# Kernel tuning notes

Hardware: AMD Instinct MI355X
Metric: run time of the kernel (lower is better)

## Reference

```python
import jax, jax.numpy as jnp
import numpy as np

B, S, E, H, FF, NQ = 8, 2048, 768, 96, 3072, 128
D_K = E // H  # 8
EPS = 1e-5


def _layernorm(x, g, b):
    m = jnp.mean(x, axis=-1, keepdims=True)
    v = jnp.mean(jnp.square(x - m), axis=-1, keepdims=True)
    return (x - m) * jax.lax.rsqrt(v + EPS) * g + b


def setup_inputs() -> dict:
    key = jax.random.key(0)
    ks = jax.random.split(key, 6)
    sc = 0.02
    return {
        "x": jax.random.normal(ks[0], (B, S, E), jnp.float32),
        "Wp": jax.random.normal(ks[1], (E, E), jnp.float32) * sc,
        "theta_rx": jax.random.normal(ks[2], (E,), jnp.float32) * sc,
        "theta_ry": jax.random.normal(ks[3], (NQ,), jnp.float32) * sc,
        "W1": jax.random.normal(ks[4], (FF, NQ), jnp.float32) * sc,
        "b1": jnp.zeros((FF,), jnp.float32),
        "W2": jax.random.normal(ks[5], (E, FF), jnp.float32) * sc,
        "b2": jnp.zeros((E,), jnp.float32),
        "ln1_g": jnp.ones((E,), jnp.float32),
        "ln1_b": jnp.zeros((E,), jnp.float32),
        "ln2_g": jnp.ones((E,), jnp.float32),
        "ln2_b": jnp.zeros((E,), jnp.float32),
    }


def reference(x, Wp, theta_rx, theta_ry, W1, b1, W2, b2, ln1_g, ln1_b, ln2_g, ln2_b):
    # --- QAttention ---
    proj = jnp.einsum('bse,fe->bsf', x, Wp)            # nn.Linear(E,E,bias=False)
    # RX(x) then RX(theta) on |0>, <Z> = cos(x+theta): batched across tokens
    qa = jnp.cos(proj + theta_rx)                      # [B,S,E]
    scores = jnp.einsum('bsd,btd->bst', qa, qa) / jnp.sqrt(jnp.float32(D_K))
    attn = jax.nn.softmax(scores, axis=-1)             # dropout=0 (eval)
    attn_out = jnp.einsum('bst,btd->bsd', attn, qa)    # [B,S,E]
    x1 = _layernorm(x + attn_out, ln1_g, ln1_b)
    # --- QFeedForward ---
    # RY(x) then RY(theta) on |0>, <Z> = cos(x+theta); encoder reads first NQ feats
    qf = jnp.cos(x1[..., :NQ] + theta_ry)              # [B,S,NQ]
    h = jax.nn.relu(jnp.einsum('bsq,fq->bsf', qf, W1) + b1)
    ffn_out = jnp.einsum('bsf,ef->bse', h, W2) + b2
    return _layernorm(x1 + ffn_out, ln2_g, ln2_b)
```

## Files before the change

kernel.cpp:

```cpp
#include <hip/hip_runtime.h>
#include <hip/hip_bf16.h>
#include <cstdio>
#include <cstdint>

typedef __bf16 bf16x8 __attribute__((ext_vector_type(8)));
typedef unsigned short u16;
typedef u16 u16x8 __attribute__((ext_vector_type(8)));
typedef float f32x4 __attribute__((ext_vector_type(4)));

#define DEV __device__ __forceinline__

static constexpr int B_ = 8, S_ = 2048, E_ = 768, NQ_ = 128, FF_ = 3072;
static constexpr int BS_ = B_ * S_;

DEV u16 f2b(float f) {
    unsigned u = __builtin_bit_cast(unsigned, f);
    unsigned r = (u + 0x7fffu + ((u >> 16) & 1u)) >> 16;
    return (u16)r;
}

#define GLD16(gp, lp) __builtin_amdgcn_global_load_lds( \
    (const __attribute__((address_space(1))) void*)(gp), \
    (__attribute__((address_space(3))) void*)(lp), 16, 0, 0)

__global__ void cvt_bf16(const float* __restrict__ in, u16* __restrict__ out, int n)
{
    const int stride = gridDim.x * blockDim.x * 4;
    for (int i = (blockIdx.x * blockDim.x + threadIdx.x) * 4; i < n; i += stride) {
        const float4 f = *(const float4*)(in + i);
        ushort4 u;
        u.x = f2b(f.x); u.y = f2b(f.y); u.z = f2b(f.z); u.w = f2b(f.w);
        *(ushort4*)(out + i) = u;
    }
}

template<int K>
DEV void kstage(const u16* A, const u16* Bm, u16* As, u16* Bs,
                int m0, int n0, int k0, int w, int t)
{
    #pragma unroll
    for (int r = 0; r < 4; ++r) {
        const int ci = r * 512 + t;
        const int row = ci >> 3;
        const int colb = ((ci & 7) * 16) ^ ((row & 7) << 4);
        GLD16(A  + (size_t)(m0 + row) * K + k0 + (colb >> 1),
              As + (size_t)(r * 512 + w * 64) * 8);
        GLD16(Bm + (size_t)(n0 + row) * K + k0 + (colb >> 1),
              Bs + (size_t)(r * 512 + w * 64) * 8);
    }
}

template<bool FIRST>
DEV void kcompute(const u16* As, const u16* Bs, f32x4 (&acc)[8][4],
                  int wr, int wc, int lane)
{
    #pragma unroll
    for (int kk = 0; kk < 2; ++kk) {
        bf16x8 af[8], bf[4];
        const int cb = kk * 64 + ((lane >> 4) << 4);
        #pragma unroll
        for (int m = 0; m < 8; ++m) {
            const int row = wr * 128 + m * 16 + (lane & 15);
            af[m] = *(const bf16x8*)((const char*)As + row * 128 + (cb ^ ((row & 7) << 4)));
        }
        #pragma unroll
        for (int n = 0; n < 4; ++n) {
            const int row = wc * 64 + n * 16 + (lane & 15);
            bf[n] = *(const bf16x8*)((const char*)Bs + row * 128 + (cb ^ ((row & 7) << 4)));
        }
        #pragma unroll
        for (int m = 0; m < 8; ++m)
            #pragma unroll
            for (int n = 0; n < 4; ++n) {
                if (FIRST && kk == 0)
                    asm("v_mfma_f32_16x16x32_bf16 %0, %1, %2, 0"
                        : "=a"(acc[m][n]) : "v"(af[m]), "v"(bf[n]));
                else
                    asm("v_mfma_f32_16x16x32_bf16 %0, %1, %2, %0"
                        : "+a"(acc[m][n]) : "v"(af[m]), "v"(bf[n]));
            }
    }
}

template<int K, int MODE>
__global__ __launch_bounds__(512, 2)
void gemm_bt(const u16* __restrict__ A, const u16* __restrict__ Bm,
             const float* __restrict__ bias, void* __restrict__ out, int N,
             size_t sA, size_t sB, size_t sC)
{
    __shared__ u16 lds[4 * 256 * 64];
    const int t = threadIdx.x;
    const int w = t >> 6, lane = t & 63;
    const int m0 = blockIdx.x * 256, n0 = blockIdx.y * 256;
    const int wr = w >> 2, wc = w & 3;
    A  += (size_t)blockIdx.z * sA;
    Bm += (size_t)blockIdx.z * sB;
    u16*   ob16 = (u16*)out   + (size_t)blockIdx.z * sC;
    float* of32 = (float*)out + (size_t)blockIdx.z * sC;
    f32x4 acc[8][4];

    kstage<K>(A, Bm, lds, lds + 16384, m0, n0, 0, w, t);
    __syncthreads();
    int cur = 0;
    for (int k0 = 0; k0 < K; k0 += 64) {
        const int nxt = cur ^ 32768;
        if (k0 + 64 < K)
            kstage<K>(A, Bm, lds + nxt, lds + nxt + 16384, m0, n0, k0 + 64, w, t);
        if (k0 == 0) kcompute<true >(lds + cur, lds + cur + 16384, acc, wr, wc, lane);
        else         kcompute<false>(lds + cur, lds + cur + 16384, acc, wr, wc, lane);
        __syncthreads();
        cur = nxt;
    }

    __builtin_amdgcn_sched_barrier(0);
    asm volatile("s_nop 7\n\ts_nop 7");
    __builtin_amdgcn_sched_barrier(0);

    #pragma unroll
    for (int m = 0; m < 8; ++m) {
        const int rowb = m0 + wr * 128 + m * 16 + ((lane >> 4) << 2);
        #pragma unroll
        for (int n = 0; n < 4; ++n) {
            const int col = n0 + wc * 64 + n * 16 + (lane & 15);
            float bv = 0.f;
            if (MODE == 0 || MODE == 1 || MODE == 2) bv = bias[col];
            #pragma unroll
            for (int r = 0; r < 4; ++r) {
                const float c = acc[m][n][r];
                const size_t idx = (size_t)(rowb + r) * N + col;
                if (MODE == 0)      ob16[idx] = f2b(__cosf(c + bv));
                else if (MODE == 1) ob16[idx] = f2b(fmaxf(c + bv, 0.f));
                else if (MODE == 2) of32[idx] = c + bv;
                else if (MODE == 3) of32[idx] = c;
                else                of32[idx] = c * 0.35355339059327373f;
            }
        }
    }
}

__global__ __launch_bounds__(256)
void transpose_bf16(const u16* __restrict__ in, u16* __restrict__ outp)
{
    __shared__ u16 tile[64][72];
    const int b = blockIdx.z;
    const int s0 = blockIdx.x * 64, d0 = blockIdx.y * 64;
    const int t = threadIdx.x;
    const u16* src = in + ((size_t)b * S_ + s0) * E_ + d0;
    #pragma unroll
    for (int i = 0; i < 2; ++i) {
        const int r = (t >> 3) + i * 32;
        const int c = (t & 7) * 8;
        u16x8 v = *(const u16x8*)(src + (size_t)r * E_ + c);
        #pragma unroll
        for (int e = 0; e < 8; ++e) tile[r][c + e] = v[e];
    }
    __syncthreads();
    u16* dst = outp + ((size_t)b * E_ + d0) * S_ + s0;
    #pragma unroll
    for (int i = 0; i < 2; ++i) {
        const int r = (t >> 3) + i * 32;
        const int c = (t & 7) * 8;
        u16x8 v;
        #pragma unroll
        for (int e = 0; e < 8; ++e) v[e] = tile[c + e][r];
        *(u16x8*)(dst + (size_t)r * S_ + c) = v;
    }
}

__global__ __launch_bounds__(256)
void softmax_rows(const float* __restrict__ s, u16* __restrict__ pout)
{
    const int t = threadIdx.x;
    const float* row = s + (size_t)blockIdx.x * (size_t)S_;
    float f[8];
    {
        const float4 a = *(const float4*)(row + t * 8);
        const float4 b = *(const float4*)(row + t * 8 + 4);
        f[0] = a.x; f[1] = a.y; f[2] = a.z; f[3] = a.w;
        f[4] = b.x; f[5] = b.y; f[6] = b.z; f[7] = b.w;
    }
    float mx = f[0];
    #pragma unroll
    for (int e = 1; e < 8; ++e) mx = fmaxf(mx, f[e]);
    #pragma unroll
    for (int d = 1; d < 64; d <<= 1) mx = fmaxf(mx, __shfl_xor(mx, d));
    __shared__ float sh[8];
    if ((t & 63) == 0) sh[t >> 6] = mx;
    __syncthreads();
    mx = fmaxf(fmaxf(sh[0], sh[1]), fmaxf(sh[2], sh[3]));
    float sum = 0.f;
    #pragma unroll
    for (int e = 0; e < 8; ++e) { f[e] = __expf(f[e] - mx); sum += f[e]; }
    #pragma unroll
    for (int d = 1; d < 64; d <<= 1) sum += __shfl_xor(sum, d);
    if ((t & 63) == 0) sh[4 + (t >> 6)] = sum;
    __syncthreads();
    sum = sh[4] + sh[5] + sh[6] + sh[7];
    const float inv = 1.f / sum;
    u16x8 v;
    #pragma unroll
    for (int e = 0; e < 8; ++e) v[e] = f2b(f[e] * inv);
    *(u16x8*)(pout + (size_t)blockIdx.x * (size_t)S_ + t * 8) = v;
}

__global__ __launch_bounds__(256)
void ln_fuse(const float* __restrict__ a, const float* __restrict__ res,
             const float* __restrict__ g, const float* __restrict__ bb,
             const float* __restrict__ theta, float* __restrict__ out,
             u16* __restrict__ qf)
{
    const int row = blockIdx.x, t = threadIdx.x;
    const float* ar = a + (size_t)row * E_;
    const float* rr = res + (size_t)row * E_;
    float v0 = ar[t] + rr[t];
    float v1 = ar[t + 256] + rr[t + 256];
    float v2 = ar[t + 512] + rr[t + 512];
    float s1 = v0 + v1 + v2;
    float s2 = v0 * v0 + v1 * v1 + v2 * v2;
    #pragma unroll
    for (int d = 1; d < 64; d <<= 1) { s1 += __shfl_xor(s1, d); s2 += __shfl_xor(s2, d); }
    __shared__ float sh[8];
    if ((t & 63) == 0) { sh[t >> 6] = s1; sh[4 + (t >> 6)] = s2; }
    __syncthreads();
    s1 = sh[0] + sh[1] + sh[2] + sh[3];
    s2 = sh[4] + sh[5] + sh[6] + sh[7];
    const float mean = s1 * (1.f / 768.f);
    const float var = s2 * (1.f / 768.f) - mean * mean;
    const float rs = rsqrtf(var + 1e-5f);
    float* orow = out + (size_t)row * E_;
    const float y0 = (v0 - mean) * rs * g[t] + bb[t];
    const float y1 = (v1 - mean) * rs * g[t + 256] + bb[t + 256];
    const float y2 = (v2 - mean) * rs * g[t + 512] + bb[t + 512];
    orow[t] = y0; orow[t + 256] = y1; orow[t + 512] = y2;
    if (qf != nullptr && t < NQ_)
        qf[(size_t)row * NQ_ + t] = f2b(cosf(y0 + theta[t]));
}

extern "C" void kernel_launch(void* const* d_in, const int* in_sizes, int n_in,
                              void* d_out, int out_size, void* d_ws, size_t ws_size,
                              hipStream_t stream)
{
    (void)in_sizes; (void)n_in; (void)out_size;
    const float* x    = (const float*)d_in[0];
    const float* Wp   = (const float*)d_in[1];
    const float* trx  = (const float*)d_in[2];
    const float* try_ = (const float*)d_in[3];
    const float* W1   = (const float*)d_in[4];
    const float* b1   = (const float*)d_in[5];
    const float* W2   = (const float*)d_in[6];
    const float* b2   = (const float*)d_in[7];
    const float* g1   = (const float*)d_in[8];
    const float* bb1  = (const float*)d_in[9];
    const float* g2   = (const float*)d_in[10];
    const float* bb2  = (const float*)d_in[11];
    float* out = (float*)d_out;

    const size_t MiB = (size_t)1 << 20;
    char* arena = (char*)d_ws;
    u16*   x_b    = (u16*)  (arena + 0);
    u16*   Wp_b   = (u16*)  (arena + 24 * MiB);
    u16*   qa     = (u16*)  (arena + 128 * MiB);
    u16*   qaT    = (u16*)  (arena + 192 * MiB);
    float* scores = (float*)(arena + 0);
    u16*   probs  = (u16*)  (arena + 128 * MiB);
    float* ao     = (float*)(arena + 0);
    float* x1     = (float*)(arena + 144 * MiB);
    u16*   qf     = (u16*)  (arena + 192 * MiB);
    u16*   h      = (u16*)  (arena + 48 * MiB);
    u16*   W1_b   = (u16*)  (arena + 216 * MiB);
    u16*   W2_b   = (u16*)  (arena + 216 * MiB + (size_t)FF_ * NQ_ * 2);
    const size_t need = 216 * MiB + (size_t)FF_ * NQ_ * 2 + (size_t)E_ * FF_ * 2;
    if (need > ws_size) {
        fprintf(stderr, "kernel_launch: ws too small: need=%zu have=%zu\n", need, ws_size);
        return;
    }

    cvt_bf16<<<512, 256, 0, stream>>>(x,  x_b,  BS_ * E_);
    cvt_bf16<<<64,  256, 0, stream>>>(Wp, Wp_b, E_ * E_);
    cvt_bf16<<<64,  256, 0, stream>>>(W1, W1_b, FF_ * NQ_);
    cvt_bf16<<<64,  256, 0, stream>>>(W2, W2_b, E_ * FF_);

    gemm_bt<E_, 0><<<dim3(BS_ / 256, E_ / 256), 512, 0, stream>>>(
        x_b, Wp_b, trx, qa, E_, 0, 0, 0);
    transpose_bf16<<<dim3(S_ / 64, E_ / 64, B_), 256, 0, stream>>>(qa, qaT);
    gemm_bt<E_, 4><<<dim3(S_ / 256, S_ / 256, B_), 512, 0, stream>>>(
        qa, qa, nullptr, scores, S_,
        (size_t)S_ * E_, (size_t)S_ * E_, (size_t)S_ * S_);
    softmax_rows<<<BS_, 256, 0, stream>>>(scores, probs);
    gemm_bt<S_, 3><<<dim3(S_ / 256, E_ / 256, B_), 512, 0, stream>>>(
        probs, qaT, nullptr, ao, E_,
        (size_t)S_ * S_, (size_t)E_ * S_, (size_t)S_ * E_);

    ln_fuse<<<BS_, 256, 0, stream>>>(ao, x, g1, bb1, try_, x1, qf);
    gemm_bt<NQ_, 1><<<dim3(BS_ / 256, FF_ / 256), 512, 0, stream>>>(
        qf, W1_b, b1, h, FF_, 0, 0, 0);
    gemm_bt<FF_, 2><<<dim3(BS_ / 256, E_ / 256), 512, 0, stream>>>(
        h, W2_b, b2, ao, E_, 0, 0, 0);
    ln_fuse<<<BS_, 256, 0, stream>>>(ao, x1, g2, bb2, nullptr, out, nullptr);
}
```

Baseline: 415.1 us.

## Switch GEMM mainloop to triple-buffered BK=32 stages with explicit vmcnt waits

Replaces the double-buffered BK=64 LDS pipeline with a three-stage ring of BK=32 tiles. Prefetch runs two stages ahead, and explicit s_waitcnt vmcnt(4) lets the next stage's global-to-LDS loads stay in flight. The swizzle is redone for 64-byte rows. LDS use drops from 128KB to 96KB per block, which may help occupancy. The cost is two barriers per half-size k-step, which doubles synchronisation relative to the MFMA work done between barriers.

```diff
diff --git a/kernel.cpp b/kernel.cpp
--- a/kernel.cpp
+++ b/kernel.cpp
@@ -35,51 +35,51 @@
 }
 
 template<int K>
-DEV void kstage(const u16* A, const u16* Bm, u16* As, u16* Bs,
-                int m0, int n0, int k0, int w, int t)
-{
-    #pragma unroll
-    for (int r = 0; r < 4; ++r) {
+DEV void kstage32(const u16* A, const u16* Bm, u16* As, u16* Bs,
+                  int m0, int n0, int k0, int w, int t)
+{
+    #pragma unroll
+    for (int r = 0; r < 2; ++r) {
         const int ci = r * 512 + t;
-        const int row = ci >> 3;
-        const int colb = ((ci & 7) * 16) ^ ((row & 7) << 4);
-        GLD16(A  + (size_t)(m0 + row) * K + k0 + (colb >> 1),
+        const int row = ci >> 2;
+        const int sw = (row & 3) ^ ((row >> 2) & 3);
+        const int cu = ((ci & 3) ^ sw) * 8;
+        GLD16(A  + (size_t)(m0 + row) * K + k0 + cu,
               As + (size_t)(r * 512 + w * 64) * 8);
-        GLD16(Bm + (size_t)(n0 + row) * K + k0 + (colb >> 1),
+        GLD16(Bm + (size_t)(n0 + row) * K + k0 + cu,
               Bs + (size_t)(r * 512 + w * 64) * 8);
     }
 }
 
 template<bool FIRST>
-DEV void kcompute(const u16* As, const u16* Bs, f32x4 (&acc)[8][4],
-                  int wr, int wc, int lane)
-{
-    #pragma unroll
-    for (int kk = 0; kk < 2; ++kk) {
-        bf16x8 af[8], bf[4];
-        const int cb = kk * 64 + ((lane >> 4) << 4);
-        #pragma unroll
-        for (int m = 0; m < 8; ++m) {
-            const int row = wr * 128 + m * 16 + (lane & 15);
-            af[m] = *(const bf16x8*)((const char*)As + row * 128 + (cb ^ ((row & 7) << 4)));
-        }
+DEV void kcompute32(const u16* As, const u16* Bs, f32x4 (&acc)[8][4],
+                    int wr, int wc, int lane)
+{
+    bf16x8 af[8], bf[4];
+    const int cb = (lane >> 4) << 4;
+    #pragma unroll
+    for (int m = 0; m < 8; ++m) {
+        const int row = wr * 128 + m * 16 + (lane & 15);
+        const int sw = ((row & 3) ^ ((row >> 2) & 3)) << 4;
+        af[m] = *(const bf16x8*)((const char*)As + row * 64 + (cb ^ sw));
+    }
+    #pragma unroll
+    for (int n = 0; n < 4; ++n) {
+        const int row = wc * 64 + n * 16 + (lane & 15);
+        const int sw = ((row & 3) ^ ((row >> 2) & 3)) << 4;
+        bf[n] = *(const bf16x8*)((const char*)Bs + row * 64 + (cb ^ sw));
+    }
+    #pragma unroll
+    for (int m = 0; m < 8; ++m)
         #pragma unroll
         for (int n = 0; n < 4; ++n) {
-            const int row = wc * 64 + n * 16 + (lane & 15);
-            bf[n] = *(const bf16x8*)((const char*)Bs + row * 128 + (cb ^ ((row & 7) << 4)));
+            if (FIRST)
+                asm("v_mfma_f32_16x16x32_bf16 %0, %1, %2, 0"
+                    : "=a"(acc[m][n]) : "v"(af[m]), "v"(bf[n]));
+            else
+                asm("v_mfma_f32_16x16x32_bf16 %0, %1, %2, %0"
+                    : "+a"(acc[m][n]) : "v"(af[m]), "v"(bf[n]));
         }
-        #pragma unroll
-        for (int m = 0; m < 8; ++m)
-            #pragma unroll
-            for (int n = 0; n < 4; ++n) {
-                if (FIRST && kk == 0)
-                    asm("v_mfma_f32_16x16x32_bf16 %0, %1, %2, 0"
-                        : "=a"(acc[m][n]) : "v"(af[m]), "v"(bf[n]));
-                else
-                    asm("v_mfma_f32_16x16x32_bf16 %0, %1, %2, %0"
-                        : "+a"(acc[m][n]) : "v"(af[m]), "v"(bf[n]));
-            }
-    }
 }
 
 template<int K, int MODE>
@@ -88,7 +88,7 @@
              const float* __restrict__ bias, void* __restrict__ out, int N,
              size_t sA, size_t sB, size_t sC)
 {
-    __shared__ u16 lds[4 * 256 * 64];
+    __shared__ u16 lds[3 * 16384];
     const int t = threadIdx.x;
     const int w = t >> 6, lane = t & 63;
     const int m0 = blockIdx.x * 256, n0 = blockIdx.y * 256;
@@ -99,17 +99,31 @@
     float* of32 = (float*)out + (size_t)blockIdx.z * sC;
     f32x4 acc[8][4];
 
-    kstage<K>(A, Bm, lds, lds + 16384, m0, n0, 0, w, t);
-    __syncthreads();
-    int cur = 0;
-    for (int k0 = 0; k0 < K; k0 += 64) {
-        const int nxt = cur ^ 32768;
-        if (k0 + 64 < K)
-            kstage<K>(A, Bm, lds + nxt, lds + nxt + 16384, m0, n0, k0 + 64, w, t);
-        if (k0 == 0) kcompute<true >(lds + cur, lds + cur + 16384, acc, wr, wc, lane);
-        else         kcompute<false>(lds + cur, lds + cur + 16384, acc, wr, wc, lane);
-        __syncthreads();
-        cur = nxt;
+    const int NS = K / 32;
+    kstage32<K>(A, Bm, lds,         lds + 8192,         m0, n0, 0,  w, t);
+    kstage32<K>(A, Bm, lds + 16384, lds + 16384 + 8192, m0, n0, 32, w, t);
+    asm volatile("s_waitcnt vmcnt(4)" ::: "memory");
+    __builtin_amdgcn_s_barrier();
+    __builtin_amdgcn_sched_barrier(0);
+
+    for (int s = 0; s < NS; ++s) {
+        const int cur = (s % 3) * 16384;
+        if (s + 2 < NS) {
+            const int nx2 = ((s + 2) % 3) * 16384;
+            kstage32<K>(A, Bm, lds + nx2, lds + nx2 + 8192,
+                        m0, n0, (s + 2) * 32, w, t);
+        }
+        if (s == 0) kcompute32<true >(lds + cur, lds + cur + 8192, acc, wr, wc, lane);
+        else        kcompute32<false>(lds + cur, lds + cur + 8192, acc, wr, wc, lane);
+        __builtin_amdgcn_sched_barrier(0);
+        asm volatile("s_waitcnt lgkmcnt(0)" ::: "memory");
+        __builtin_amdgcn_s_barrier();
+        if (s + 2 < NS)
+            asm volatile("s_waitcnt vmcnt(4)" ::: "memory");
+        else
+            asm volatile("s_waitcnt vmcnt(0)" ::: "memory");
+        __builtin_amdgcn_s_barrier();
+        __builtin_amdgcn_sched_barrier(0);
     }
 
     __builtin_amdgcn_sched_barrier(0);
```

Result: slower. 438.4 us (+5.6%).

## Shrink GEMM tiles to 128x128 single-buffered, keep 256 tile for W1 GEMM

Applied to the files above, without the earlier changes.

The generic GEMM now uses 128x128 tiles with 4 waves, 256 threads and single-buffered LDS with two barriers per k-step, replacing the 256x256 double-buffered design. It is used for the Wp, QK^T, PV and W2 GEMMs. A copy of the old 256-tile kernel is kept only for the short-K W1 GEMM. The goal is more blocks and better occupancy and tail balance on small grids, at the cost of less reuse per tile and no overlap of global loads with MFMA work.

```diff
diff --git a/kernel.cpp b/kernel.cpp
--- a/kernel.cpp
+++ b/kernel.cpp
@@ -40,27 +40,27 @@
 {
     #pragma unroll
     for (int r = 0; r < 4; ++r) {
-        const int ci = r * 512 + t;
+        const int ci = r * 256 + t;
         const int row = ci >> 3;
         const int colb = ((ci & 7) * 16) ^ ((row & 7) << 4);
         GLD16(A  + (size_t)(m0 + row) * K + k0 + (colb >> 1),
-              As + (size_t)(r * 512 + w * 64) * 8);
+              As + (size_t)(r * 256 + w * 64) * 8);
         GLD16(Bm + (size_t)(n0 + row) * K + k0 + (colb >> 1),
-              Bs + (size_t)(r * 512 + w * 64) * 8);
+              Bs + (size_t)(r * 256 + w * 64) * 8);
     }
 }
 
 template<bool FIRST>
-DEV void kcompute(const u16* As, const u16* Bs, f32x4 (&acc)[8][4],
+DEV void kcompute(const u16* As, const u16* Bs, f32x4 (&acc)[4][4],
                   int wr, int wc, int lane)
 {
     #pragma unroll
     for (int kk = 0; kk < 2; ++kk) {
-        bf16x8 af[8], bf[4];
+        bf16x8 af[4], bf[4];
         const int cb = kk * 64 + ((lane >> 4) << 4);
         #pragma unroll
-        for (int m = 0; m < 8; ++m) {
-            const int row = wr * 128 + m * 16 + (lane & 15);
+        for (int m = 0; m < 4; ++m) {
+            const int row = wr * 64 + m * 16 + (lane & 15);
             af[m] = *(const bf16x8*)((const char*)As + row * 128 + (cb ^ ((row & 7) << 4)));
         }
         #pragma unroll
@@ -69,7 +69,7 @@
             bf[n] = *(const bf16x8*)((const char*)Bs + row * 128 + (cb ^ ((row & 7) << 4)));
         }
         #pragma unroll
-        for (int m = 0; m < 8; ++m)
+        for (int m = 0; m < 4; ++m)
             #pragma unroll
             for (int n = 0; n < 4; ++n) {
                 if (FIRST && kk == 0)
@@ -83,33 +83,29 @@
 }
 
 template<int K, int MODE>
-__global__ __launch_bounds__(512, 2)
+__global__ __launch_bounds__(256, 3)
 void gemm_bt(const u16* __restrict__ A, const u16* __restrict__ Bm,
              const float* __restrict__ bias, void* __restrict__ out, int N,
              size_t sA, size_t sB, size_t sC)
 {
-    __shared__ u16 lds[4 * 256 * 64];
+    __shared__ u16 As[128 * 64];
+    __shared__ u16 Bs[128 * 64];
     const int t = threadIdx.x;
     const int w = t >> 6, lane = t & 63;
-    const int m0 = blockIdx.x * 256, n0 = blockIdx.y * 256;
-    const int wr = w >> 2, wc = w & 3;
+    const int m0 = blockIdx.x * 128, n0 = blockIdx.y * 128;
+    const int wr = w >> 1, wc = w & 1;
     A  += (size_t)blockIdx.z * sA;
     Bm += (size_t)blockIdx.z * sB;
     u16*   ob16 = (u16*)out   + (size_t)blockIdx.z * sC;
     float* of32 = (float*)out + (size_t)blockIdx.z * sC;
-    f32x4 acc[8][4];
-
-    kstage<K>(A, Bm, lds, lds + 16384, m0, n0, 0, w, t);
-    __syncthreads();
-    int cur = 0;
+    f32x4 acc[4][4];
+
     for (int k0 = 0; k0 < K; k0 += 64) {
-        const int nxt = cur ^ 32768;
-        if (k0 + 64 < K)
-            kstage<K>(A, Bm, lds + nxt, lds + nxt + 16384, m0, n0, k0 + 64, w, t);
-        if (k0 == 0) kcompute<true >(lds + cur, lds + cur + 16384, acc, wr, wc, lane);
-        else         kcompute<false>(lds + cur, lds + cur + 16384, acc, wr, wc, lane);
         __syncthreads();
-        cur = nxt;
+        kstage<K>(A, Bm, As, Bs, m0, n0, k0, w, t);
+        __syncthreads();
+        if (k0 == 0) kcompute<true >(As, Bs, acc, wr, wc, lane);
+        else         kcompute<false>(As, Bs, acc, wr, wc, lane);
     }
 
     __builtin_amdgcn_sched_barrier(0);
@@ -117,8 +113,8 @@
     __builtin_amdgcn_sched_barrier(0);
 
     #pragma unroll
-    for (int m = 0; m < 8; ++m) {
-        const int rowb = m0 + wr * 128 + m * 16 + ((lane >> 4) << 2);
+    for (int m = 0; m < 4; ++m) {
+        const int rowb = m0 + wr * 64 + m * 16 + ((lane >> 4) << 2);
         #pragma unroll
         for (int n = 0; n < 4; ++n) {
             const int col = n0 + wc * 64 + n * 16 + (lane & 15);
@@ -133,6 +129,100 @@
                 else if (MODE == 2) of32[idx] = c + bv;
                 else if (MODE == 3) of32[idx] = c;
                 else                of32[idx] = c * 0.35355339059327373f;
+            }
+        }
+    }
+}
+
+template<int K>
+DEV void kstage256(const u16* A, const u16* Bm, u16* As, u16* Bs,
+                   int m0, int n0, int k0, int w, int t)
+{
+    #pragma unroll
+    for (int r = 0; r < 4; ++r) {
+        const int ci = r * 512 + t;
+        const int row = ci >> 3;
+        const int colb = ((ci & 7) * 16) ^ ((row & 7) << 4);
+        GLD16(A  + (size_t)(m0 + row) * K + k0 + (colb >> 1),
+              As + (size_t)(r * 512 + w * 64) * 8);
+        GLD16(Bm + (size_t)(n0 + row) * K + k0 + (colb >> 1),
+              Bs + (size_t)(r * 512 + w * 64) * 8);
+    }
+}
+
+template<bool FIRST>
+DEV void kcompute256(const u16* As, const u16* Bs, f32x4 (&acc)[8][4],
+                     int wr, int wc, int lane)
+{
+    #pragma unroll
+    for (int kk = 0; kk < 2; ++kk) {
+        bf16x8 af[8], bf[4];
+        const int cb = kk * 64 + ((lane >> 4) << 4);
+        #pragma unroll
+        for (int m = 0; m < 8; ++m) {
+            const int row = wr * 128 + m * 16 + (lane & 15);
+            af[m] = *(const bf16x8*)((const char*)As + row * 128 + (cb ^ ((row & 7) << 4)));
+        }
+        #pragma unroll
+        for (int n = 0; n < 4; ++n) {
+            const int row = wc * 64 + n * 16 + (lane & 15);
+            bf[n] = *(const bf16x8*)((const char*)Bs + row * 128 + (cb ^ ((row & 7) << 4)));
+        }
+        #pragma unroll
+        for (int m = 0; m < 8; ++m)
+            #pragma unroll
+            for (int n = 0; n < 4; ++n) {
+                if (FIRST && kk == 0)
+                    asm("v_mfma_f32_16x16x32_bf16 %0, %1, %2, 0"
+                        : "=a"(acc[m][n]) : "v"(af[m]), "v"(bf[n]));
+                else
+                    asm("v_mfma_f32_16x16x32_bf16 %0, %1, %2, %0"
+                        : "+a"(acc[m][n]) : "v"(af[m]), "v"(bf[n]));
+            }
+    }
+}
+
+template<int K, int MODE>
+__global__ __launch_bounds__(512, 2)
+void gemm_bt256(const u16* __restrict__ A, const u16* __restrict__ Bm,
+                const float* __restrict__ bias, void* __restrict__ out, int N)
+{
+    __shared__ u16 lds[4 * 256 * 64];
+    const int t = threadIdx.x;
+    const int w = t >> 6, lane = t & 63;
+    const int m0 = blockIdx.x * 256, n0 = blockIdx.y * 256;
+    const int wr = w >> 2, wc = w & 3;
+    u16* ob16 = (u16*)out;
+    f32x4 acc[8][4];
+
+    kstage256<K>(A, Bm, lds, lds + 16384, m0, n0, 0, w, t);
+    __syncthreads();
+    int cur = 0;
+    for (int k0 = 0; k0 < K; k0 += 64) {
+        const int nxt = cur ^ 32768;
+        if (k0 + 64 < K)
+            kstage256<K>(A, Bm, lds + nxt, lds + nxt + 16384, m0, n0, k0 + 64, w, t);
+        if (k0 == 0) kcompute256<true >(lds + cur, lds + cur + 16384, acc, wr, wc, lane);
+        else         kcompute256<false>(lds + cur, lds + cur + 16384, acc, wr, wc, lane);
+        __syncthreads();
+        cur = nxt;
+    }
+
+    __builtin_amdgcn_sched_barrier(0);
+    asm volatile("s_nop 7\n\ts_nop 7");
+    __builtin_amdgcn_sched_barrier(0);
+
+    #pragma unroll
+    for (int m = 0; m < 8; ++m) {
+        const int rowb = m0 + wr * 128 + m * 16 + ((lane >> 4) << 2);
+        #pragma unroll
+        for (int n = 0; n < 4; ++n) {
+            const int col = n0 + wc * 64 + n * 16 + (lane & 15);
+            const float bv = bias[col];
+            #pragma unroll
+            for (int r = 0; r < 4; ++r) {
+                const float c = acc[m][n][r];
+                ob16[(size_t)(rowb + r) * N + col] = f2b(fmaxf(c + bv, 0.f));
             }
         }
     }
@@ -280,21 +370,21 @@
     cvt_bf16<<<64,  256, 0, stream>>>(W1, W1_b, FF_ * NQ_);
     cvt_bf16<<<64,  256, 0, stream>>>(W2, W2_b, E_ * FF_);
 
-    gemm_bt<E_, 0><<<dim3(BS_ / 256, E_ / 256), 512, 0, stream>>>(
+    gemm_bt<E_, 0><<<dim3(BS_ / 128, E_ / 128), 256, 0, stream>>>(
         x_b, Wp_b, trx, qa, E_, 0, 0, 0);
     transpose_bf16<<<dim3(S_ / 64, E_ / 64, B_), 256, 0, stream>>>(qa, qaT);
-    gemm_bt<E_, 4><<<dim3(S_ / 256, S_ / 256, B_), 512, 0, stream>>>(
+    gemm_bt<E_, 4><<<dim3(S_ / 128, S_ / 128, B_), 256, 0, stream>>>(
         qa, qa, nullptr, scores, S_,
         (size_t)S_ * E_, (size_t)S_ * E_, (size_t)S_ * S_);
     softmax_rows<<<BS_, 256, 0, stream>>>(scores, probs);
-    gemm_bt<S_, 3><<<dim3(S_ / 256, E_ / 256, B_), 512, 0, stream>>>(
+    gemm_bt<S_, 3><<<dim3(S_ / 128, E_ / 128, B_), 256, 0, stream>>>(
         probs, qaT, nullptr, ao, E_,
         (size_t)S_ * S_, (size_t)E_ * S_, (size_t)S_ * E_);
 
     ln_fuse<<<BS_, 256, 0, stream>>>(ao, x, g1, bb1, try_, x1, qf);
-    gemm_bt<NQ_, 1><<<dim3(BS_ / 256, FF_ / 256), 512, 0, stream>>>(
-        qf, W1_b, b1, h, FF_, 0, 0, 0);
-    gemm_bt<FF_, 2><<<dim3(BS_ / 256, E_ / 256), 512, 0, stream>>>(
+    gemm_bt256<NQ_, 1><<<dim3(BS_ / 256, FF_ / 256), 512, 0, stream>>>(
+        qf, W1_b, b1, h, FF_);
+    gemm_bt<FF_, 2><<<dim3(BS_ / 128, E_ / 128), 256, 0, stream>>>(
         h, W2_b, b2, ao, E_, 0, 0, 0);
     ln_fuse<<<BS_, 256, 0, stream>>>(ao, x1, g2, bb2, nullptr, out, nullptr);
 }
```

Measured after the change: 409.9 us. Within noise of the previous version (-1.2%).
